# Kernel optimization log

Hardware: AMD Instinct MI355X
Metric: run time of the kernel (lower is better)

## Reference

```python
import jax, jax.numpy as jnp
import numpy as np

N_HEADS = 16


def setup_inputs() -> dict:
    key = jax.random.key(0)
    ks = jax.random.split(key, 11)
    B, S, D = 8, 1024, 1024
    scale = 1.0 / np.sqrt(D)
    inp = {
        "batch": jax.random.normal(ks[0], (B, S, D), jnp.float32),
        "lengths": jax.random.randint(ks[1], (B,), 1, S + 1, jnp.int32),
        "wq": jax.random.normal(ks[2], (D, D), jnp.float32) * scale,
        "bq": jax.random.normal(ks[3], (D,), jnp.float32) * 0.02,
        "wk": jax.random.normal(ks[4], (D, D), jnp.float32) * scale,
        "bk": jax.random.normal(ks[5], (D,), jnp.float32) * 0.02,
        "wv": jax.random.normal(ks[6], (D, D), jnp.float32) * scale,
        "bv": jax.random.normal(ks[7], (D,), jnp.float32) * 0.02,
        "w0": jax.random.normal(ks[8], (D, D), jnp.float32) * scale,
        "b0": jax.random.normal(ks[9], (D,), jnp.float32) * 0.02,
    }
    return inp


def reference(batch, lengths, wq, bq, wk, bk, wv, bv, w0, b0):
    B, S, D = batch.shape
    H = N_HEADS
    dk = D // H
    q = (batch @ wq + bq).reshape(B, S, H, dk)
    k = (batch @ wk + bk).reshape(B, S, H, dk)
    v = (batch @ wv + bv).reshape(B, S, H, dk)
    # scores[b,h,s,q] = q_s . k_q  (no 1/sqrt(d_k) scaling, as in original)
    scores = jnp.einsum('bshd,bqhd->bhsq', q, k)
    rows = jnp.arange(S)[:, None]
    cols = jnp.arange(S)[None, :]
    causal = cols >= rows + 1                                   # [S,S]
    pad = jnp.arange(S)[None, :] >= lengths[:, None]            # [B,S] over key axis
    mask = causal[None, None, :, :] | pad[:, None, None, :]     # [B,1->H,S,S]
    scores = jnp.where(mask, -jnp.inf, scores)
    attn = jax.nn.softmax(scores, axis=-1)                      # [B,H,S,S]
    # Original uses einsum('bhss,bshd->bshd') -> diagonal of attention matrix
    attn_diag = jnp.diagonal(attn, axis1=2, axis2=3)            # [B,H,S]
    weighted = jnp.einsum('bhs,bshd->bshd', attn_diag, v)       # [B,S,H,dk]
    concated = weighted.reshape(B, S, D)
    return concated @ w0 + b0
```

## Files before the change

kernel.cpp:

```cpp
#include <hip/hip_runtime.h>
#include <hip/hip_bf16.h>
#include <stdint.h>
#include <math.h>

typedef short short8 __attribute__((ext_vector_type(8)));
typedef float f32x4 __attribute__((ext_vector_type(4)));
typedef unsigned short u16;

__device__ __forceinline__ u16 f2bf(float f) {
    unsigned u = __float_as_uint(f);
    unsigned r = 0x7FFFu + ((u >> 16) & 1u);
    return (u16)((u + r) >> 16);
}
__device__ __forceinline__ float bf2f(u16 h) {
    return __uint_as_float((unsigned)h << 16);
}

#define GL_LDS16(g, l)                                                         \
    __builtin_amdgcn_global_load_lds(                                          \
        (const __attribute__((address_space(1))) void*)(g),                    \
        (__attribute__((address_space(3))) void*)(l), 16, 0, 0)

__global__ __launch_bounds__(256) void k_prep(
    const float* __restrict__ batch, u16* __restrict__ Ab, int nconv,
    const float* __restrict__ wq, const float* __restrict__ wk,
    const float* __restrict__ wv, const float* __restrict__ w0,
    u16* __restrict__ wcat, u16* __restrict__ w0T, int Dim) {
    __shared__ float tile[64][65];
    const int bid = blockIdx.x;
    const int t = threadIdx.x;
    if (bid < nconv) {
        int i = bid * 256 + t;
        const float4* s = (const float4*)batch + (size_t)i * 2;
        float4 a = s[0], b = s[1];
        uint4 o;
        o.x = (unsigned)f2bf(a.x) | ((unsigned)f2bf(a.y) << 16);
        o.y = (unsigned)f2bf(a.z) | ((unsigned)f2bf(a.w) << 16);
        o.z = (unsigned)f2bf(b.x) | ((unsigned)f2bf(b.y) << 16);
        o.w = (unsigned)f2bf(b.z) | ((unsigned)f2bf(b.w) << 16);
        ((uint4*)Ab)[i] = o;
        return;
    }
    const int id = bid - nconv;
    const int w = id >> 8, r = id & 255;
    const float* W = (w == 0) ? wq : (w == 1) ? wk : (w == 2) ? wv : w0;
    u16* WT = (w == 3) ? w0T : wcat + (size_t)w * Dim * Dim;
    const int k0 = (r & 15) * 64, n0 = (r >> 4) * 64;
    const int col = t & 63, rb = t >> 6;
#pragma unroll
    for (int i = 0; i < 16; ++i) {
        int rr = i * 4 + rb;
        tile[rr][col] = W[(size_t)(k0 + rr) * Dim + n0 + col];
    }
    __syncthreads();
#pragma unroll
    for (int i = 0; i < 16; ++i) {
        int rr = i * 4 + rb;
        WT[(size_t)(n0 + rr) * Dim + k0 + col] = f2bf(tile[col][rr]);
    }
}

template <int FUSED>
__global__ __launch_bounds__(512) void k_gemm8(
    const u16* __restrict__ A, const u16* __restrict__ BT,
    const float* __restrict__ b1, const float* __restrict__ b2,
    const float* __restrict__ b3,
    u16* __restrict__ Qh, u16* __restrict__ Ql,
    u16* __restrict__ Kh, u16* __restrict__ Kl,
    u16* __restrict__ Vb, float* __restrict__ C,
    int K, int ldo) {
    __shared__ __align__(16) u16 ldsbuf[36864];

    const int wg = blockIdx.x;
    const int xcd = wg & 7, idc = wg >> 3;
    const int ml = idc & 3, nbn = idc >> 2;
    const int m0 = ((xcd << 2) + ml) << 8;
    const int n0 = nbn << 7;
    const int t = threadIdx.x;
    const int lane = t & 63, wave = t >> 6;
    const int wr = wave >> 1, wc = wave & 1;
    const int r16 = lane & 15, kq = lane >> 4;
    const int nt = K >> 6;
    const int np = nt << 1;

    int offA[4], offB[4];
#pragma unroll
    for (int mi = 0; mi < 4; ++mi) {
        int row = wr * 64 + mi * 16 + r16;
        offA[mi] = row * 32 + ((kq ^ ((row >> 1) & 3)) << 3);
    }
#pragma unroll
    for (int n = 0; n < 4; ++n) {
        int row = wc * 64 + n * 16 + r16;
        offB[n] = row * 32 + ((kq ^ ((row >> 1) & 3)) << 3);
    }

    f32x4 acc[4][4];
#pragma unroll
    for (int m = 0; m < 4; ++m)
#pragma unroll
        for (int n = 0; n < 4; ++n) acc[m][n] = (f32x4){0.f, 0.f, 0.f, 0.f};

    auto stage = [&](int h) {
        const int buf = h % 3;
        const int kt = ((h >> 1) << 6) + ((h & 1) << 5);
        u16* Abase = ldsbuf + buf * 12288;
        u16* Bbase = ldsbuf + buf * 12288 + 8192;
#pragma unroll
        for (int r = 0; r < 2; ++r) {
            int li = (r << 9) + t;
            int row = li >> 2;
            int kk = ((li & 3) ^ ((row >> 1) & 3)) << 3;
            GL_LDS16(A + (size_t)(m0 + row) * K + kt + kk,
                     Abase + ((li & ~63) << 3));
        }
        {
            int li = t;
            int row = li >> 2;
            int kk = ((li & 3) ^ ((row >> 1) & 3)) << 3;
            GL_LDS16(BT + (size_t)(n0 + row) * K + kt + kk,
                     Bbase + ((li & ~63) << 3));
        }
    };

    stage(0);
    stage(1);

    for (int p = 0; p < np; ++p) {
        if (p + 1 < np)
            asm volatile("s_waitcnt vmcnt(3)" ::: "memory");
        else
            asm volatile("s_waitcnt vmcnt(0)" ::: "memory");
        __builtin_amdgcn_sched_barrier(0);
        __builtin_amdgcn_s_barrier();
        __builtin_amdgcn_sched_barrier(0);

        const u16* base = ldsbuf + (p % 3) * 12288;
        short8 a[4], bfr[4];
#pragma unroll
        for (int mi = 0; mi < 4; ++mi)
            a[mi] = *(const short8*)(base + offA[mi]);
#pragma unroll
        for (int n = 0; n < 4; ++n)
            bfr[n] = *(const short8*)(base + 8192 + offB[n]);

        if (p + 2 < np) stage(p + 2);

        asm volatile("s_waitcnt lgkmcnt(0)" ::: "memory");
        __builtin_amdgcn_sched_barrier(0);
        __builtin_amdgcn_s_setprio(1);
#pragma unroll
        for (int mi = 0; mi < 4; ++mi)
#pragma unroll
            for (int n = 0; n < 4; ++n)
                acc[mi][n] = __builtin_amdgcn_mfma_f32_16x16x32_bf16(
                    a[mi], bfr[n], acc[mi][n], 0, 0, 0);
        __builtin_amdgcn_s_setprio(0);
        __builtin_amdgcn_sched_barrier(0);
    }

    if (FUSED) {
        const int seg = n0 >> 10;
        const float* bias = (seg == 0) ? b1 : (seg == 1) ? b2 : b3;
        u16* oh = (seg == 0) ? Qh : (seg == 1) ? Kh : Vb;
        u16* ol = (seg == 0) ? Ql : Kl;
        const int nc0 = n0 & 1023;
        const int nplanes = (seg < 2) ? 2 : 1;
        u16* lds = ldsbuf;
        for (int p = 0; p < nplanes; ++p) {
            __syncthreads();
#pragma unroll
            for (int n = 0; n < 4; ++n) {
                int col = wc * 64 + n * 16 + r16;
                float bvv = bias[nc0 + col];
#pragma unroll
                for (int mi = 0; mi < 4; ++mi) {
                    int row = wr * 64 + mi * 16 + kq * 4;
#pragma unroll
                    for (int j = 0; j < 4; ++j) {
                        float val = acc[mi][n][j] + bvv;
                        u16 hi = f2bf(val);
                        u16 w = p ? f2bf(val - bf2f(hi)) : hi;
                        lds[(row + j) * 128 + col] = w;
                    }
                }
            }
            __syncthreads();
            u16* dst = p ? ol : oh;
#pragma unroll
            for (int i = 0; i < 8; ++i) {
                int li = (i << 9) + t;
                int row = li >> 4, ch = li & 15;
                short8 v = *(const short8*)&lds[row * 128 + ch * 8];
                *(short8*)(dst + (size_t)(m0 + row) * ldo + nc0 + ch * 8) = v;
            }
        }
    } else {
#pragma unroll
        for (int n = 0; n < 4; ++n) {
            int col = n0 + wc * 64 + n * 16 + r16;
            float bvv = b1[col];
#pragma unroll
            for (int mi = 0; mi < 4; ++mi) {
                int row = m0 + wr * 64 + mi * 16 + kq * 4;
#pragma unroll
                for (int j = 0; j < 4; ++j)
                    C[(size_t)(row + j) * ldo + col] = acc[mi][n][j] + bvv;
            }
        }
    }
}

__global__ __launch_bounds__(256, 2) void k_scores(
    const u16* __restrict__ Qhi, const u16* __restrict__ Qlo,
    const u16* __restrict__ Khi, const u16* __restrict__ Klo,
    const u16* __restrict__ Vb, const int* __restrict__ lengths,
    u16* __restrict__ Wt, int S, int D) {
    __shared__ __align__(16) u16 KsHi[2][4096];
    __shared__ __align__(16) u16 KsLo[2][4096];
    __shared__ float dbuf[128];

    const int wg = blockIdx.x;
    const int xcd = wg & 7, idc = wg >> 3;
    const int bh = (xcd << 4) + (idc >> 3);
    const int bx = idc & 7;
    const int b = bh >> 4, h = bh & 15;
    const int nchunk = S >> 6;
    const int a0 = bx << 6;
    const int b0 = (nchunk - 1 - bx) << 6;

    const int t = threadIdx.x;
    const int lane = t & 63, wave = t >> 6;
    const int r16 = lane & 15, h2 = lane >> 4;
    const int len = lengths[b];

    short8 qh[2][2], ql[2][2];
#pragma unroll
    for (int m = 0; m < 2; ++m) {
        const int qm = m ? b0 : a0;
        const int row = qm + (wave << 4) + r16;
#pragma unroll
        for (int ks = 0; ks < 2; ++ks) {
            size_t off = ((size_t)(b * S) + row) * D + (h << 6) + (ks << 5) + (h2 << 3);
            qh[m][ks] = *(const short8*)(Qhi + off);
            ql[m][ks] = *(const short8*)(Qlo + off);
        }
    }

    float sum[2][4];
    float diag[2] = {-1e30f, -1e30f};
#pragma unroll
    for (int m = 0; m < 2; ++m)
#pragma unroll
        for (int r = 0; r < 4; ++r) sum[m][r] = 0.f;

    auto stage_k = [&](int j0, int bufi) {
#pragma unroll
        for (int p = 0; p < 2; ++p) {
            const int base_row = p * 32 + wave * 8;
            const int row = base_row + (lane >> 3);
            const int lc = (lane & 7) ^ (row & 7);
            size_t g = ((size_t)(b * S) + j0 + row) * D + (h << 6) + (lc << 3);
            GL_LDS16(Khi + g, &KsHi[bufi][base_row * 64]);
            GL_LDS16(Klo + g, &KsLo[bufi][base_row * 64]);
        }
    };

    const int jmax = min(b0 + 63, len - 1);
    stage_k(0, 0);
    for (int j0 = 0; j0 <= jmax; j0 += 64) {
        const int tb = (j0 >> 6) & 1;
        asm volatile("s_waitcnt vmcnt(0)" ::: "memory");
        __builtin_amdgcn_sched_barrier(0);
        __builtin_amdgcn_s_barrier();
        __builtin_amdgcn_sched_barrier(0);
        if (j0 + 64 <= jmax) stage_k(j0 + 64, tb ^ 1);

        f32x4 acc[2][4];
#pragma unroll
        for (int m = 0; m < 2; ++m)
#pragma unroll
            for (int n = 0; n < 4; ++n) acc[m][n] = (f32x4){0.f, 0.f, 0.f, 0.f};

#pragma unroll
        for (int ks = 0; ks < 2; ++ks) {
            short8 kh[4], kl[4];
#pragma unroll
            for (int n = 0; n < 4; ++n) {
                int row = (n << 4) + r16;
                int lc = (ks << 2) + h2;
                int phys = (row << 7) + ((lc ^ (row & 7)) << 4);
                kh[n] = *(const short8*)((const char*)&KsHi[tb][0] + phys);
                kl[n] = *(const short8*)((const char*)&KsLo[tb][0] + phys);
            }
#pragma unroll
            for (int m = 0; m < 2; ++m) {
                const int qm = m ? b0 : a0;
                if (j0 > qm) continue;
#pragma unroll
                for (int n = 0; n < 4; ++n) {
                    if (j0 + (n << 4) > qm + (wave << 4) + 15) continue;
                    acc[m][n] = __builtin_amdgcn_mfma_f32_16x16x32_bf16(qh[m][ks], kh[n], acc[m][n], 0, 0, 0);
                    acc[m][n] = __builtin_amdgcn_mfma_f32_16x16x32_bf16(qh[m][ks], kl[n], acc[m][n], 0, 0, 0);
                    acc[m][n] = __builtin_amdgcn_mfma_f32_16x16x32_bf16(ql[m][ks], kh[n], acc[m][n], 0, 0, 0);
                }
            }
        }

        const bool pad = (j0 + 64 > len);
#pragma unroll
        for (int m = 0; m < 2; ++m) {
            const int qm = m ? b0 : a0;
            if (j0 > qm) continue;
            const bool causal = (j0 == qm);
            if (causal || pad) {
#pragma unroll
                for (int n = 0; n < 4; ++n)
#pragma unroll
                    for (int r = 0; r < 4; ++r) {
                        int j = j0 + (n << 4) + r16;
                        int s = qm + (wave << 4) + (h2 << 2) + r;
                        if (j > s || j >= len) acc[m][n][r] = -1e30f;
                    }
                if (causal) {
#pragma unroll
                    for (int r = 0; r < 4; ++r)
                        if (r16 == (h2 << 2) + r) {
#pragma unroll
                            for (int n = 0; n < 4; ++n)
                                if (n == wave) diag[m] = acc[m][n][r];
                        }
                }
            }
#pragma unroll
            for (int r = 0; r < 4; ++r)
                sum[m][r] += __expf(acc[m][0][r]) + __expf(acc[m][1][r]) +
                             __expf(acc[m][2][r]) + __expf(acc[m][3][r]);
        }
    }

#pragma unroll
    for (int m = 0; m < 2; ++m)
#pragma unroll
        for (int r = 0; r < 4; ++r) {
            float sv = sum[m][r];
            sv += __shfl_xor(sv, 1);
            sv += __shfl_xor(sv, 2);
            sv += __shfl_xor(sv, 4);
            sv += __shfl_xor(sv, 8);
            sum[m][r] = sv;
        }

#pragma unroll
    for (int m = 0; m < 2; ++m)
#pragma unroll
        for (int r = 0; r < 4; ++r)
            if (r16 == (h2 << 2) + r)
                dbuf[(m << 6) + (wave << 4) + r16] = __expf(diag[m]) / sum[m][r];
    __syncthreads();

#pragma unroll
    for (int i = 0; i < 8; ++i) {
        int ri = i * 16 + (t >> 4);
        int c4 = (t & 15) << 2;
        int srow = (ri < 64) ? a0 + ri : b0 + ri - 64;
        float dv = dbuf[ri];
        const uint2 vv = *(const uint2*)(Vb + ((size_t)(b * S) + srow) * D + (h << 6) + c4);
        float x0 = bf2f((u16)(vv.x & 0xffffu)), x1 = bf2f((u16)(vv.x >> 16));
        float x2 = bf2f((u16)(vv.y & 0xffffu)), x3 = bf2f((u16)(vv.y >> 16));
        uint2 o;
        o.x = (unsigned)f2bf(x0 * dv) | ((unsigned)f2bf(x1 * dv) << 16);
        o.y = (unsigned)f2bf(x2 * dv) | ((unsigned)f2bf(x3 * dv) << 16);
        *(uint2*)(Wt + ((size_t)(b * S) + srow) * D + (h << 6) + c4) = o;
    }
}

extern "C" void kernel_launch(void* const* d_in, const int* in_sizes, int n_in,
                              void* d_out, int out_size, void* d_ws, size_t ws_size,
                              hipStream_t stream) {
    const float* batch = (const float*)d_in[0];
    const int* lengths = (const int*)d_in[1];
    const float* wq = (const float*)d_in[2];
    const float* bq = (const float*)d_in[3];
    const float* wk = (const float*)d_in[4];
    const float* bk = (const float*)d_in[5];
    const float* wv = (const float*)d_in[6];
    const float* bv = (const float*)d_in[7];
    const float* w0 = (const float*)d_in[8];
    const float* b0 = (const float*)d_in[9];

    const int D = in_sizes[3];
    const int B = in_sizes[1];
    const int S = in_sizes[0] / (B * D);
    const int H = 16;
    const int M = B * S;

    char* ws = (char*)d_ws;
    u16* Ab = (u16*)ws;    ws += (size_t)M * D * 2;
    u16* wcat = (u16*)ws;  ws += (size_t)3 * D * D * 2;
    u16* w0T = (u16*)ws;   ws += (size_t)D * D * 2;
    u16* Qhi = (u16*)ws;   ws += (size_t)M * D * 2;
    u16* Qlo = (u16*)ws;   ws += (size_t)M * D * 2;
    u16* Khi = (u16*)ws;   ws += (size_t)M * D * 2;
    u16* Klo = (u16*)ws;   ws += (size_t)M * D * 2;
    u16* Vb = (u16*)ws;    ws += (size_t)M * D * 2;
    u16* Wtb = (u16*)ws;   ws += (size_t)M * D * 2;

    const int nconv = M * D / 8 / 256;
    k_prep<<<nconv + 4 * (D / 64) * (D / 64), 256, 0, stream>>>(
        batch, Ab, nconv, wq, wk, wv, w0, wcat, w0T, D);

    k_gemm8<1><<<(M / 256) * (3 * D / 128), 512, 0, stream>>>(
        Ab, wcat, bq, bk, bv, Qhi, Qlo, Khi, Klo, Vb, nullptr, D, D);

    k_scores<<<(S / 128) * H * B, 256, 0, stream>>>(Qhi, Qlo, Khi, Klo, Vb,
                                                    lengths, Wtb, S, D);

    k_gemm8<0><<<(M / 256) * (D / 128), 512, 0, stream>>>(
        Wtb, w0T, b0, nullptr, nullptr, nullptr, nullptr, nullptr, nullptr, nullptr,
        (float*)d_out, D, D);
}
```

Measured before the change: 152.1 us.

## Use 256x256 tile GEMM with split-K-half pipelining for fused QKV projection

Replaces the templated 256x128 GEMM for the fused Q/K/V projection with a dedicated kernel using 256x256 output tiles. Each of 8 waves computes a 128x64 sub-tile, and loads are staged per 32-wide K half into double-buffered LDS. The bigger tile is meant to raise data reuse per global load and cut the total number of A and B tile fetches. In exchange it uses 128KB of LDS, which limits occupancy to one block per CU, and leaves fewer blocks (384) to balance across CUs. The output projection keeps the old kernel under a new non-templated name.

```diff
diff --git a/kernel.cpp b/kernel.cpp
--- a/kernel.cpp
+++ b/kernel.cpp
@@ -60,14 +60,159 @@
     }
 }
 
-template <int FUSED>
-__global__ __launch_bounds__(512) void k_gemm8(
+__global__ __launch_bounds__(512, 2) void k_gemmfat(
     const u16* __restrict__ A, const u16* __restrict__ BT,
     const float* __restrict__ b1, const float* __restrict__ b2,
     const float* __restrict__ b3,
     u16* __restrict__ Qh, u16* __restrict__ Ql,
     u16* __restrict__ Kh, u16* __restrict__ Kl,
-    u16* __restrict__ Vb, float* __restrict__ C,
+    u16* __restrict__ Vb, int K, int ldo) {
+    __shared__ __align__(16) u16 ldsbuf[65536];
+
+    const int wg = blockIdx.x;
+    const int xcd = wg & 7, idc = wg >> 3;
+    const int ml = idc & 3, nbn = idc >> 2;
+    const int m0 = ((xcd << 2) + ml) << 8;
+    const int n0 = nbn << 8;
+    const int tid = threadIdx.x;
+    const int lane = tid & 63, wave = tid >> 6;
+    const int wr = wave >> 2, wc = wave & 3;
+    const int r16 = lane & 15, kq = lane >> 4;
+    const int nt = K >> 6;
+
+    int offA[2][4], offB[4];
+#pragma unroll
+    for (int mh = 0; mh < 2; ++mh)
+#pragma unroll
+        for (int mi = 0; mi < 4; ++mi) {
+            int row = mh * 64 + mi * 16 + r16;
+            offA[mh][mi] = row * 32 + ((kq ^ ((row >> 1) & 3)) << 3);
+        }
+#pragma unroll
+    for (int n = 0; n < 4; ++n) {
+        int row = wc * 64 + n * 16 + r16;
+        offB[n] = row * 32 + ((kq ^ ((row >> 1) & 3)) << 3);
+    }
+
+    f32x4 acc[8][4];
+#pragma unroll
+    for (int m = 0; m < 8; ++m)
+#pragma unroll
+        for (int n = 0; n < 4; ++n) acc[m][n] = (f32x4){0.f, 0.f, 0.f, 0.f};
+
+    auto stageA = [&](int tn, int u, int kh) {
+        u16* base = ldsbuf + (tn & 1) * 16384 + kh * 8192 + u * 4096;
+        int row = tid >> 2;
+        int kk = ((tid & 3) ^ ((row >> 1) & 3)) << 3;
+        GL_LDS16(A + (size_t)(m0 + u * 128 + row) * K + (tn << 6) + kh * 32 + kk,
+                 base + ((tid & ~63) << 3));
+    };
+    auto stageB = [&](int tn, int kh) {
+        u16* base = ldsbuf + 32768 + (tn & 1) * 16384 + kh * 8192;
+#pragma unroll
+        for (int r = 0; r < 2; ++r) {
+            int li = (r << 9) + tid;
+            int row = li >> 2;
+            int kk = ((li & 3) ^ ((row >> 1) & 3)) << 3;
+            GL_LDS16(BT + (size_t)(n0 + row) * K + (tn << 6) + kh * 32 + kk,
+                     base + ((li & ~63) << 3));
+        }
+    };
+
+    stageB(0, 0); stageA(0, 0, 0); stageA(0, 1, 0);
+    stageB(0, 1); stageA(0, 0, 1); stageA(0, 1, 1);
+
+    for (int tl = 0; tl < nt; ++tl) {
+        const int buf = tl & 1;
+#pragma unroll
+        for (int kh = 0; kh < 2; ++kh) {
+            if (kh == 0 || tl + 1 < nt)
+                asm volatile("s_waitcnt vmcnt(4)" ::: "memory");
+            else
+                asm volatile("s_waitcnt vmcnt(0)" ::: "memory");
+            __builtin_amdgcn_sched_barrier(0);
+            __builtin_amdgcn_s_barrier();
+            __builtin_amdgcn_sched_barrier(0);
+
+            const u16* Abase = ldsbuf + buf * 16384 + kh * 8192 + wr * 4096;
+            const u16* Bbase = ldsbuf + 32768 + buf * 16384 + kh * 8192;
+            short8 a[4], bfr[4];
+#pragma unroll
+            for (int n = 0; n < 4; ++n)
+                bfr[n] = *(const short8*)(Bbase + offB[n]);
+#pragma unroll
+            for (int mi = 0; mi < 4; ++mi)
+                a[mi] = *(const short8*)(Abase + offA[0][mi]);
+            if (tl + 1 < nt) { stageB(tl + 1, kh); stageA(tl + 1, 0, kh); }
+            asm volatile("s_waitcnt lgkmcnt(0)" ::: "memory");
+            __builtin_amdgcn_sched_barrier(0);
+            __builtin_amdgcn_s_setprio(1);
+#pragma unroll
+            for (int mi = 0; mi < 4; ++mi)
+#pragma unroll
+                for (int n = 0; n < 4; ++n)
+                    acc[mi][n] = __builtin_amdgcn_mfma_f32_16x16x32_bf16(
+                        a[mi], bfr[n], acc[mi][n], 0, 0, 0);
+            __builtin_amdgcn_s_setprio(0);
+            __builtin_amdgcn_sched_barrier(0);
+
+#pragma unroll
+            for (int mi = 0; mi < 4; ++mi)
+                a[mi] = *(const short8*)(Abase + offA[1][mi]);
+            if (tl + 1 < nt) stageA(tl + 1, 1, kh);
+            asm volatile("s_waitcnt lgkmcnt(0)" ::: "memory");
+            __builtin_amdgcn_sched_barrier(0);
+            __builtin_amdgcn_s_setprio(1);
+#pragma unroll
+            for (int mi = 0; mi < 4; ++mi)
+#pragma unroll
+                for (int n = 0; n < 4; ++n)
+                    acc[4 + mi][n] = __builtin_amdgcn_mfma_f32_16x16x32_bf16(
+                        a[mi], bfr[n], acc[4 + mi][n], 0, 0, 0);
+            __builtin_amdgcn_s_setprio(0);
+            __builtin_amdgcn_sched_barrier(0);
+        }
+    }
+
+    const int seg = n0 >> 10;
+    const float* bias = (seg == 0) ? b1 : (seg == 1) ? b2 : b3;
+    u16* oh = (seg == 0) ? Qh : (seg == 1) ? Kh : Vb;
+    u16* ol = (seg == 0) ? Ql : Kl;
+    const int nc0 = n0 & 1023;
+    const int nplanes = (seg < 2) ? 2 : 1;
+    for (int p = 0; p < nplanes; ++p) {
+        __syncthreads();
+#pragma unroll
+        for (int n = 0; n < 4; ++n) {
+            int col = wc * 64 + n * 16 + r16;
+            float bvv = bias[nc0 + col];
+#pragma unroll
+            for (int mi = 0; mi < 8; ++mi) {
+                int row = wr * 128 + mi * 16 + kq * 4;
+#pragma unroll
+                for (int j = 0; j < 4; ++j) {
+                    float val = acc[mi][n][j] + bvv;
+                    u16 hi = f2bf(val);
+                    u16 w = p ? f2bf(val - bf2f(hi)) : hi;
+                    ldsbuf[(row + j) * 256 + col] = w;
+                }
+            }
+        }
+        __syncthreads();
+        u16* dst = p ? ol : oh;
+#pragma unroll
+        for (int i = 0; i < 16; ++i) {
+            int li = (i << 9) + tid;
+            int row = li >> 5, ch = li & 31;
+            short8 v = *(const short8*)&ldsbuf[row * 256 + ch * 8];
+            *(short8*)(dst + (size_t)(m0 + row) * ldo + nc0 + ch * 8) = v;
+        }
+    }
+}
+
+__global__ __launch_bounds__(512) void k_gemmthin(
+    const u16* __restrict__ A, const u16* __restrict__ BT,
+    const float* __restrict__ b1, float* __restrict__ C,
     int K, int ldo) {
     __shared__ __align__(16) u16 ldsbuf[36864];
 
@@ -159,54 +304,16 @@
         __builtin_amdgcn_sched_barrier(0);
     }
 
-    if (FUSED) {
-        const int seg = n0 >> 10;
-        const float* bias = (seg == 0) ? b1 : (seg == 1) ? b2 : b3;
-        u16* oh = (seg == 0) ? Qh : (seg == 1) ? Kh : Vb;
-        u16* ol = (seg == 0) ? Ql : Kl;
-        const int nc0 = n0 & 1023;
-        const int nplanes = (seg < 2) ? 2 : 1;
-        u16* lds = ldsbuf;
-        for (int p = 0; p < nplanes; ++p) {
-            __syncthreads();
-#pragma unroll
-            for (int n = 0; n < 4; ++n) {
-                int col = wc * 64 + n * 16 + r16;
-                float bvv = bias[nc0 + col];
-#pragma unroll
-                for (int mi = 0; mi < 4; ++mi) {
-                    int row = wr * 64 + mi * 16 + kq * 4;
-#pragma unroll
-                    for (int j = 0; j < 4; ++j) {
-                        float val = acc[mi][n][j] + bvv;
-                        u16 hi = f2bf(val);
-                        u16 w = p ? f2bf(val - bf2f(hi)) : hi;
-                        lds[(row + j) * 128 + col] = w;
-                    }
-                }
-            }
-            __syncthreads();
-            u16* dst = p ? ol : oh;
-#pragma unroll
-            for (int i = 0; i < 8; ++i) {
-                int li = (i << 9) + t;
-                int row = li >> 4, ch = li & 15;
-                short8 v = *(const short8*)&lds[row * 128 + ch * 8];
-                *(short8*)(dst + (size_t)(m0 + row) * ldo + nc0 + ch * 8) = v;
-            }
-        }
-    } else {
-#pragma unroll
-        for (int n = 0; n < 4; ++n) {
-            int col = n0 + wc * 64 + n * 16 + r16;
-            float bvv = b1[col];
-#pragma unroll
-            for (int mi = 0; mi < 4; ++mi) {
-                int row = m0 + wr * 64 + mi * 16 + kq * 4;
-#pragma unroll
-                for (int j = 0; j < 4; ++j)
-                    C[(size_t)(row + j) * ldo + col] = acc[mi][n][j] + bvv;
-            }
+#pragma unroll
+    for (int n = 0; n < 4; ++n) {
+        int col = n0 + wc * 64 + n * 16 + r16;
+        float bvv = b1[col];
+#pragma unroll
+        for (int mi = 0; mi < 4; ++mi) {
+            int row = m0 + wr * 64 + mi * 16 + kq * 4;
+#pragma unroll
+            for (int j = 0; j < 4; ++j)
+                C[(size_t)(row + j) * ldo + col] = acc[mi][n][j] + bvv;
         }
     }
 }
@@ -410,13 +517,12 @@
     k_prep<<<nconv + 4 * (D / 64) * (D / 64), 256, 0, stream>>>(
         batch, Ab, nconv, wq, wk, wv, w0, wcat, w0T, D);
 
-    k_gemm8<1><<<(M / 256) * (3 * D / 128), 512, 0, stream>>>(
-        Ab, wcat, bq, bk, bv, Qhi, Qlo, Khi, Klo, Vb, nullptr, D, D);
+    k_gemmfat<<<(M / 256) * (3 * D / 256), 512, 0, stream>>>(
+        Ab, wcat, bq, bk, bv, Qhi, Qlo, Khi, Klo, Vb, D, D);
 
     k_scores<<<(S / 128) * H * B, 256, 0, stream>>>(Qhi, Qlo, Khi, Klo, Vb,
                                                     lengths, Wtb, S, D);
 
-    k_gemm8<0><<<(M / 256) * (D / 128), 512, 0, stream>>>(
-        Wtb, w0T, b0, nullptr, nullptr, nullptr, nullptr, nullptr, nullptr, nullptr,
-        (float*)d_out, D, D);
-}
+    k_gemmthin<<<(M / 256) * (D / 128), 512, 0, stream>>>(
+        Wtb, w0T, b0, (float*)d_out, D, D);
+}
```

Result: slower. 177.6 us (+16.8%).
